# Kernel optimization log

Measured on AMD Instinct MI355X. Metric: run time of the kernel, lower is better.

Reference implementation:

```python
import jax, jax.numpy as jnp
import numpy as np

N, L, P = 8192, 20, 30          # obstacles, observation_len, pred_len
E, H, C = 64, 128, 2048         # embed_size, hidden_size, cnn_out_size (resnet50)


def setup_inputs() -> dict:
    key = jax.random.key(0)
    ks = jax.random.split(key, 10)
    rn = lambda k, s, sc=1.0: jax.random.normal(k, s, jnp.float32) * sc
    return {
        "img_embedding": rn(ks[0], (N, C)),
        "obs_pos": rn(ks[1], (N, L, 2)),
        "obs_pos_rel": rn(ks[2], (N, L, 2), 0.1),
        "obs_hist_size": jax.random.randint(ks[3], (N,), 0, L, jnp.int32),
        "h0": rn(ks[4], (H,), 0.1),
        "W_embed": rn(ks[5], (2, E), 0.5),
        "b_embed": jnp.zeros((E,), jnp.float32),
        "W_ih": rn(ks[6], (E, 4 * H), 1.0 / np.sqrt(E)),
        "W_hh": rn(ks[7], (H, 4 * H), 1.0 / np.sqrt(H)),
        "b_ih": jnp.zeros((4 * H,), jnp.float32),
        "b_hh": jnp.zeros((4 * H,), jnp.float32),
        "W_pred": rn(ks[8], (H + C, 2), 1.0 / np.sqrt(H + C)),
        "b_pred": jnp.zeros((2,), jnp.float32),
    }


def _forward(img_embedding, obs_pos, obs_pos_rel, obs_hist_size, h0,
             W_embed, b_embed, W_ih, W_hh, b_ih, b_hh, W_pred, b_pred):
    n, l, _ = obs_pos.shape
    hid = h0.shape[0]
    h = jnp.broadcast_to(h0, (n, hid))
    c = h  # original code initializes BOTH ht and ct from h0 (faithful to source)

    def lstm_cell(h, c, rel):
        # disp_embed (Linear(2,E)+ReLU) followed by a single LSTM step, PyTorch gate order i,f,g,o
        e = jax.nn.relu(rel @ W_embed + b_embed)            # [n, E]
        g = e @ W_ih + h @ W_hh + (b_ih + b_hh)             # [n, 4H]
        i, f, gg, o = jnp.split(g, 4, axis=-1)
        c_new = jax.nn.sigmoid(f) * c + jax.nn.sigmoid(i) * jnp.tanh(gg)
        h_new = jax.nn.sigmoid(o) * jnp.tanh(c_new)
        return h_new, c_new

    # ---- observation phase: t = 1 .. l-1, masked state update ----
    thresh = l - jnp.arange(1, l)                           # [l-1]
    masks = obs_hist_size[None, :] > thresh[:, None]        # [l-1, n] bool
    rels = jnp.swapaxes(obs_pos_rel[:, 1:, :], 0, 1)        # [l-1, n, 2]

    def obs_step(carry, x):
        h, c = carry
        rel, m = x
        h_new, c_new = lstm_cell(h, c, rel)
        m = m[:, None]
        return (jnp.where(m, h_new, h), jnp.where(m, c_new, c)), None

    (h, c), _ = jax.lax.scan(obs_step, (h, c), (rels, masks))

    # ---- prediction phase: pred_mask == all ones ----
    # pred_layer(cat(ht, img_emb)) == ht @ Wp_h + (img_emb @ Wp_img + b); the image
    # part is loop-invariant so hoist it (same math, far less memory traffic).
    img_proj = img_embedding @ W_pred[hid:] + b_pred        # [n, 2]
    Wp_h = W_pred[:hid]                                     # [H, 2]

    def pred_step(carry, _):
        h, c, pos = carry
        rel = h @ Wp_h + img_proj                           # pred_out[:, t-L]
        pos = pos + rel                                     # pred_traj[:, t-L]
        h_new, c_new = lstm_cell(h, c, rel)
        return (h_new, c_new, pos), pos

    _, traj = jax.lax.scan(pred_step, (h, c, obs_pos[:, -1, :]), None, length=P)
    return jnp.swapaxes(traj, 0, 1)                         # [n, P, 2]


def reference(img_embedding, obs_pos, obs_pos_rel, obs_hist_size, h0,
              W_embed, b_embed, W_ih, W_hh, b_ih, b_hh, W_pred, b_pred):
    return _forward(img_embedding, obs_pos, obs_pos_rel, obs_hist_size, h0,
                    W_embed, b_embed, W_ih, W_hh, b_ih, b_hh, W_pred, b_pred)
```

## Files before the change

kernel.cpp:

```cpp
#include <hip/hip_runtime.h>

typedef float f32x4 __attribute__((ext_vector_type(4)));
typedef float f32x2 __attribute__((ext_vector_type(2)));
typedef short bf16x8 __attribute__((ext_vector_type(8)));

#define N_TOT 8192
#define L_OBS 20
#define P_PRED 30
#define E_DIM 64
#define H_DIM 128
#define C_DIM 2048
#define G_DIM 512
#define M_ROWS 32
#define NTH 512
#define A_PAD 200

#define K1 1.442695041f
#define K2 2.885390082f

static __device__ __forceinline__ unsigned short f2bf(float f) {
  union { float f; unsigned int u; } v; v.f = f;
  unsigned int u = v.u;
  return (unsigned short)((u + 0x7FFFu + ((u >> 16) & 1u)) >> 16);
}
static __device__ __forceinline__ float bf2f(unsigned short b) {
  union { unsigned int u; float f; } v; v.u = ((unsigned int)b) << 16;
  return v.f;
}
static __device__ __forceinline__ float ex2(float x)  { float r; asm("v_exp_f32 %0, %1" : "=v"(r) : "v"(x)); return r; }
static __device__ __forceinline__ float rcpn(float x) { float r; asm("v_rcp_f32 %0, %1" : "=v"(r) : "v"(x)); return r; }
static __device__ __forceinline__ unsigned int cvtpk(float lo, float hi) {
  unsigned int r; asm("v_cvt_pk_bf16_f32 %0, %1, %2" : "=v"(r) : "v"(lo), "v"(hi)); return r;
}

__global__ __launch_bounds__(NTH, 2)
void lstm_traj(const float* __restrict__ img,
               const float* __restrict__ obs_pos,
               const float* __restrict__ obs_rel,
               const int*   __restrict__ hist,
               const float* __restrict__ h0,
               const float* __restrict__ W_embed,
               const float* __restrict__ b_embed,
               const float* __restrict__ W_ih,
               const float* __restrict__ W_hh,
               const float* __restrict__ b_ih,
               const float* __restrict__ b_hh,
               const float* __restrict__ W_pred,
               const float* __restrict__ b_pred,
               float* __restrict__ out)
{
  __shared__ unsigned short A_lds[2][M_ROWS][A_PAD];
  __shared__ float We_lds[2][E_DIM];
  __shared__ float be_lds[E_DIM];
  __shared__ float Wp_lds[H_DIM][2];

  const int t    = threadIdx.x;
  const int w    = t >> 6;
  const int l    = t & 63;
  const int u15  = l & 15;
  const int rq   = l >> 4;
  const int u    = w * 16 + u15;
  const int wg0  = blockIdx.x * M_ROWS;
  const int grow = t >> 4;
  const int gj   = t & 15;

  const float* relrow = obs_rel + (wg0 + grow) * (L_OBS * 2);

  if (t < 128) We_lds[t >> 6][t & 63] = W_embed[t];
  if (t < 64)  be_lds[t] = b_embed[t];
  if (t >= 128 && t < 384) ((float*)Wp_lds)[t - 128] = W_pred[t - 128];
  __syncthreads();

  bf16x8 B[4][6];
#pragma unroll
  for (int ks = 0; ks < 6; ++ks)
#pragma unroll
    for (int i = 0; i < 8; ++i) {
      const int k = ks * 32 + rq * 8 + i;
      const float* Wrow = (k < E_DIM) ? (W_ih + k * G_DIM) : (W_hh + (k - E_DIM) * G_DIM);
#pragma unroll
      for (int gt = 0; gt < 4; ++gt)
        B[gt][ks][i] = (short)f2bf(Wrow[gt * 128 + u]);
    }

  const float nbi = -K1 * (b_ih[u]       + b_hh[u]);
  const float nbf = -K1 * (b_ih[128 + u] + b_hh[128 + u]);
  const float nbg = -K2 * (b_ih[256 + u] + b_hh[256 + u]);
  const float nbo = -K1 * (b_ih[384 + u] + b_hh[384 + u]);

  const float h0u = h0[u];
  const unsigned short h0b = f2bf(h0u);
  float hf[2][4];
  float cs[2][4];
  int sact[2];
#pragma unroll
  for (int rt = 0; rt < 2; ++rt) {
    sact[rt] = 0;
#pragma unroll
    for (int q = 0; q < 4; ++q) {
      const int row = rt * 16 + rq * 4 + q;
      hf[rt][q] = h0u; cs[rt][q] = h0u;
      sact[rt] |= ((20 - hist[wg0 + row]) & 255) << (8 * q);
      A_lds[0][row][64 + u] = h0b;
    }
  }

  {
    const f32x2 rr = *(const f32x2*)(relrow + 2 * 2);
    const int j = gj * 4;
    const float e0 = fmaxf(fmaf(rr.x, We_lds[0][j],     fmaf(rr.y, We_lds[1][j],     be_lds[j])),     0.f);
    const float e1 = fmaxf(fmaf(rr.x, We_lds[0][j + 1], fmaf(rr.y, We_lds[1][j + 1], be_lds[j + 1])), 0.f);
    const float e2 = fmaxf(fmaf(rr.x, We_lds[0][j + 2], fmaf(rr.y, We_lds[1][j + 2], be_lds[j + 2])), 0.f);
    const float e3 = fmaxf(fmaf(rr.x, We_lds[0][j + 3], fmaf(rr.y, We_lds[1][j + 3], be_lds[j + 3])), 0.f);
    uint2 pk; pk.x = cvtpk(e0, e1); pk.y = cvtpk(e2, e3);
    *(uint2*)&A_lds[0][grow][j] = pk;
  }

  float pos0 = obs_pos[(wg0 + grow) * (L_OBS * 2) + (L_OBS - 1) * 2];
  float pos1 = obs_pos[(wg0 + grow) * (L_OBS * 2) + (L_OBS - 1) * 2 + 1];
  float ip0 = 0.f, ip1 = 0.f;
  {
    const float* irow = img + (long)(wg0 + grow) * C_DIM;
#pragma unroll 4
    for (int i = 0; i < 32; ++i) {
      const int k0 = i * 64 + gj * 4;
      const f32x4 v  = *(const f32x4*)(irow + k0);
      const f32x4 wa = *(const f32x4*)(W_pred + (H_DIM + k0) * 2);
      const f32x4 wb = *(const f32x4*)(W_pred + (H_DIM + k0) * 2 + 4);
      ip0 = fmaf(v.x, wa.x, fmaf(v.y, wa.z, fmaf(v.z, wb.x, fmaf(v.w, wb.z, ip0))));
      ip1 = fmaf(v.x, wa.y, fmaf(v.y, wa.w, fmaf(v.z, wb.y, fmaf(v.w, wb.w, ip1))));
    }
#pragma unroll
    for (int m = 8; m >= 1; m >>= 1) { ip0 += __shfl_xor(ip0, m); ip1 += __shfl_xor(ip1, m); }
    ip0 += b_pred[0]; ip1 += b_pred[1];
  }
  __syncthreads();

  int cur = 0;

  auto gates_and_h = [&](f32x4 (&acc)[2][4], int nxt_, int s_, bool domask) {
#pragma unroll
    for (int rt = 0; rt < 2; ++rt) {
#pragma unroll
      for (int q = 0; q < 4; ++q) {
        const float A_ = ex2(fmaf(acc[rt][0][q], -K1, nbi));
        const float F_ = ex2(fmaf(acc[rt][1][q], -K1, nbf));
        const float B_ = ex2(fmaf(acc[rt][2][q], -K2, nbg));
        const float C_ = ex2(fmaf(acc[rt][3][q], -K1, nbo));
        const float P2 = 1.f + B_;
        const float PB = (1.f + A_) * P2;
        const float Q  = 1.f + F_;
        const float cn = fmaf(cs[rt][q], PB, (2.f - P2) * Q) * rcpn(PB * Q);
        const float D_ = ex2(-K2 * cn);
        const float tc = fmaf(2.f, rcpn(1.f + D_), -1.f);
        const float hn = tc * rcpn(1.f + C_);
        bool act = true;
        if (domask) act = s_ >= ((sact[rt] >> (8 * q)) & 255);
        if (act) { cs[rt][q] = cn; hf[rt][q] = hn; }
      }
      const unsigned int p01 = cvtpk(hf[rt][0], hf[rt][1]);
      const unsigned int p23 = cvtpk(hf[rt][2], hf[rt][3]);
      const int rowb = rt * 16 + rq * 4;
      A_lds[nxt_][rowb + 0][64 + u] = (unsigned short)p01;
      A_lds[nxt_][rowb + 1][64 + u] = (unsigned short)(p01 >> 16);
      A_lds[nxt_][rowb + 2][64 + u] = (unsigned short)p23;
      A_lds[nxt_][rowb + 3][64 + u] = (unsigned short)(p23 >> 16);
    }
  };

#pragma unroll 1
  for (int s = 1; s < L_OBS - 1; ++s) {
    const int nxt = cur ^ 1;
    const int sN = (s + 2 <= L_OBS - 1) ? (s + 2) : (L_OBS - 1);
    const f32x2 rrN = *(const f32x2*)(relrow + sN * 2);

    f32x4 acc[2][4];
#pragma unroll
    for (int rt = 0; rt < 2; ++rt)
#pragma unroll
      for (int gt = 0; gt < 4; ++gt) { acc[rt][gt].x = 0.f; acc[rt][gt].y = 0.f; acc[rt][gt].z = 0.f; acc[rt][gt].w = 0.f; }
#pragma unroll
    for (int ks = 0; ks < 6; ++ks)
#pragma unroll
      for (int rt = 0; rt < 2; ++rt) {
        const bf16x8 a = *(const bf16x8*)&A_lds[cur][rt * 16 + u15][ks * 32 + rq * 8];
#pragma unroll
        for (int gt = 0; gt < 4; ++gt)
          acc[rt][gt] = __builtin_amdgcn_mfma_f32_16x16x32_bf16(a, B[gt][ks], acc[rt][gt], 0, 0, 0);
      }

    {
      const int j = gj * 4;
      const float e0 = fmaxf(fmaf(rrN.x, We_lds[0][j],     fmaf(rrN.y, We_lds[1][j],     be_lds[j])),     0.f);
      const float e1 = fmaxf(fmaf(rrN.x, We_lds[0][j + 1], fmaf(rrN.y, We_lds[1][j + 1], be_lds[j + 1])), 0.f);
      const float e2 = fmaxf(fmaf(rrN.x, We_lds[0][j + 2], fmaf(rrN.y, We_lds[1][j + 2], be_lds[j + 2])), 0.f);
      const float e3 = fmaxf(fmaf(rrN.x, We_lds[0][j + 3], fmaf(rrN.y, We_lds[1][j + 3], be_lds[j + 3])), 0.f);
      uint2 pk; pk.x = cvtpk(e0, e1); pk.y = cvtpk(e2, e3);
      *(uint2*)&A_lds[nxt][grow][j] = pk;
    }

    gates_and_h(acc, nxt, s, true);
    cur = nxt;
    __syncthreads();
  }

#pragma unroll 1
  for (int p = 0; p < P_PRED; ++p) {
    f32x4 acc[2][4];
    const bool last = (p == P_PRED - 1);
    if (!last) {
#pragma unroll
      for (int rt = 0; rt < 2; ++rt)
#pragma unroll
        for (int gt = 0; gt < 4; ++gt) { acc[rt][gt].x = 0.f; acc[rt][gt].y = 0.f; acc[rt][gt].z = 0.f; acc[rt][gt].w = 0.f; }
#pragma unroll
      for (int ks = 2; ks < 6; ++ks)
#pragma unroll
        for (int rt = 0; rt < 2; ++rt) {
          const bf16x8 a = *(const bf16x8*)&A_lds[cur][rt * 16 + u15][ks * 32 + rq * 8];
#pragma unroll
          for (int gt = 0; gt < 4; ++gt)
            acc[rt][gt] = __builtin_amdgcn_mfma_f32_16x16x32_bf16(a, B[gt][ks], acc[rt][gt], 0, 0, 0);
        }
    }

    const bf16x8 hv = *(const bf16x8*)&A_lds[cur][grow][64 + gj * 8];
    float s0 = 0.f, s1 = 0.f;
#pragma unroll
    for (int i = 0; i < 8; ++i) {
      const float hfv = bf2f((unsigned short)hv[i]);
      s0 = fmaf(hfv, Wp_lds[gj * 8 + i][0], s0);
      s1 = fmaf(hfv, Wp_lds[gj * 8 + i][1], s1);
    }
#pragma unroll
    for (int m = 8; m >= 1; m >>= 1) { s0 += __shfl_xor(s0, m); s1 += __shfl_xor(s1, m); }
    const float rel0 = s0 + ip0, rel1 = s1 + ip1;
    pos0 += rel0; pos1 += rel1;
    if (gj == 0) {
      float2 o; o.x = pos0; o.y = pos1;
      *(float2*)&out[((long)(wg0 + grow) * P_PRED + p) * 2] = o;
    }
    if (last) break;

    {
      const int j = gj * 4;
      const float e0 = fmaxf(fmaf(rel0, We_lds[0][j],     fmaf(rel1, We_lds[1][j],     be_lds[j])),     0.f);
      const float e1 = fmaxf(fmaf(rel0, We_lds[0][j + 1], fmaf(rel1, We_lds[1][j + 1], be_lds[j + 1])), 0.f);
      const float e2 = fmaxf(fmaf(rel0, We_lds[0][j + 2], fmaf(rel1, We_lds[1][j + 2], be_lds[j + 2])), 0.f);
      const float e3 = fmaxf(fmaf(rel0, We_lds[0][j + 3], fmaf(rel1, We_lds[1][j + 3], be_lds[j + 3])), 0.f);
      uint2 pk; pk.x = cvtpk(e0, e1); pk.y = cvtpk(e2, e3);
      *(uint2*)&A_lds[cur][grow][j] = pk;
    }
    __syncthreads();

#pragma unroll
    for (int ks = 0; ks < 2; ++ks)
#pragma unroll
      for (int rt = 0; rt < 2; ++rt) {
        const bf16x8 a = *(const bf16x8*)&A_lds[cur][rt * 16 + u15][ks * 32 + rq * 8];
#pragma unroll
        for (int gt = 0; gt < 4; ++gt)
          acc[rt][gt] = __builtin_amdgcn_mfma_f32_16x16x32_bf16(a, B[gt][ks], acc[rt][gt], 0, 0, 0);
      }

    const int nxt = cur ^ 1;
    gates_and_h(acc, nxt, 0, false);
    cur = nxt;
    __syncthreads();
  }
}

extern "C" void kernel_launch(void* const* d_in, const int* in_sizes, int n_in,
                              void* d_out, int out_size, void* d_ws, size_t ws_size,
                              hipStream_t stream) {
  (void)in_sizes; (void)n_in; (void)out_size; (void)d_ws; (void)ws_size;
  lstm_traj<<<dim3(N_TOT / M_ROWS), dim3(NTH), 0, stream>>>(
      (const float*)d_in[0],
      (const float*)d_in[1],
      (const float*)d_in[2],
      (const int*)  d_in[3],
      (const float*)d_in[4],
      (const float*)d_in[5],
      (const float*)d_in[6],
      (const float*)d_in[7],
      (const float*)d_in[8],
      (const float*)d_in[9],
      (const float*)d_in[10],
      (const float*)d_in[11],
      (const float*)d_in[12],
      (float*)d_out);
}
```

Baseline: 125.0 us.

## Compute prediction projection via MFMA in registers, drop mid-step barrier

The prediction-phase output projection h@Wp_h now runs as small MFMAs against a register-resident bf16 copy of W_pred, with results broadcast by ds_bpermute, instead of an LDS scalar dot plus shuffle reduction. Each wave then computes its own embedding fragments for the input part in registers. This removes the LDS write and the __syncthreads between embedding and the input-side MFMAs in every prediction step. In exchange it adds redundant per-wave embedding compute and more register pressure (wpf, ah, ef) under a 2-blocks-per-CU launch bound.

```diff
diff --git a/kernel.cpp b/kernel.cpp
--- a/kernel.cpp
+++ b/kernel.cpp
@@ -23,14 +23,13 @@
   unsigned int u = v.u;
   return (unsigned short)((u + 0x7FFFu + ((u >> 16) & 1u)) >> 16);
 }
-static __device__ __forceinline__ float bf2f(unsigned short b) {
-  union { unsigned int u; float f; } v; v.u = ((unsigned int)b) << 16;
-  return v.f;
-}
 static __device__ __forceinline__ float ex2(float x)  { float r; asm("v_exp_f32 %0, %1" : "=v"(r) : "v"(x)); return r; }
 static __device__ __forceinline__ float rcpn(float x) { float r; asm("v_rcp_f32 %0, %1" : "=v"(r) : "v"(x)); return r; }
 static __device__ __forceinline__ unsigned int cvtpk(float lo, float hi) {
   unsigned int r; asm("v_cvt_pk_bf16_f32 %0, %1, %2" : "=v"(r) : "v"(lo), "v"(hi)); return r;
+}
+static __device__ __forceinline__ float bperm16(int u15, float v) {
+  return __int_as_float(__builtin_amdgcn_ds_bpermute(u15 << 2, __float_as_int(v)));
 }
 
 __global__ __launch_bounds__(NTH, 2)
@@ -52,7 +51,7 @@
   __shared__ unsigned short A_lds[2][M_ROWS][A_PAD];
   __shared__ float We_lds[2][E_DIM];
   __shared__ float be_lds[E_DIM];
-  __shared__ float Wp_lds[H_DIM][2];
+  __shared__ float ip_lds[M_ROWS][2];
 
   const int t    = threadIdx.x;
   const int w    = t >> 6;
@@ -68,7 +67,6 @@
 
   if (t < 128) We_lds[t >> 6][t & 63] = W_embed[t];
   if (t < 64)  be_lds[t] = b_embed[t];
-  if (t >= 128 && t < 384) ((float*)Wp_lds)[t - 128] = W_pred[t - 128];
   __syncthreads();
 
   bf16x8 B[4][6];
@@ -81,6 +79,15 @@
 #pragma unroll
       for (int gt = 0; gt < 4; ++gt)
         B[gt][ks][i] = (short)f2bf(Wrow[gt * 128 + u]);
+    }
+
+  bf16x8 wpf[4];
+#pragma unroll
+  for (int ks4 = 0; ks4 < 4; ++ks4)
+#pragma unroll
+    for (int i = 0; i < 8; ++i) {
+      const int k = ks4 * 32 + rq * 8 + i;
+      wpf[ks4][i] = (u15 < 2) ? (short)f2bf(W_pred[k * 2 + u15]) : (short)0;
     }
 
   const float nbi = -K1 * (b_ih[u]       + b_hh[u]);
@@ -116,10 +123,8 @@
     *(uint2*)&A_lds[0][grow][j] = pk;
   }
 
-  float pos0 = obs_pos[(wg0 + grow) * (L_OBS * 2) + (L_OBS - 1) * 2];
-  float pos1 = obs_pos[(wg0 + grow) * (L_OBS * 2) + (L_OBS - 1) * 2 + 1];
-  float ip0 = 0.f, ip1 = 0.f;
   {
+    float ig0 = 0.f, ig1 = 0.f;
     const float* irow = img + (long)(wg0 + grow) * C_DIM;
 #pragma unroll 4
     for (int i = 0; i < 32; ++i) {
@@ -127,14 +132,21 @@
       const f32x4 v  = *(const f32x4*)(irow + k0);
       const f32x4 wa = *(const f32x4*)(W_pred + (H_DIM + k0) * 2);
       const f32x4 wb = *(const f32x4*)(W_pred + (H_DIM + k0) * 2 + 4);
-      ip0 = fmaf(v.x, wa.x, fmaf(v.y, wa.z, fmaf(v.z, wb.x, fmaf(v.w, wb.z, ip0))));
-      ip1 = fmaf(v.x, wa.y, fmaf(v.y, wa.w, fmaf(v.z, wb.y, fmaf(v.w, wb.w, ip1))));
-    }
-#pragma unroll
-    for (int m = 8; m >= 1; m >>= 1) { ip0 += __shfl_xor(ip0, m); ip1 += __shfl_xor(ip1, m); }
-    ip0 += b_pred[0]; ip1 += b_pred[1];
+      ig0 = fmaf(v.x, wa.x, fmaf(v.y, wa.z, fmaf(v.z, wb.x, fmaf(v.w, wb.z, ig0))));
+      ig1 = fmaf(v.x, wa.y, fmaf(v.y, wa.w, fmaf(v.z, wb.y, fmaf(v.w, wb.w, ig1))));
+    }
+#pragma unroll
+    for (int m = 8; m >= 1; m >>= 1) { ig0 += __shfl_xor(ig0, m); ig1 += __shfl_xor(ig1, m); }
+    if (gj == 0) { ip_lds[grow][0] = ig0 + b_pred[0]; ip_lds[grow][1] = ig1 + b_pred[1]; }
   }
   __syncthreads();
+
+  const float ipA0 = ip_lds[u15][0],      ipA1 = ip_lds[u15][1];
+  const float ipB0 = ip_lds[16 + u15][0], ipB1 = ip_lds[16 + u15][1];
+  float posA0 = obs_pos[(wg0 + u15) * (L_OBS * 2) + (L_OBS - 1) * 2];
+  float posA1 = obs_pos[(wg0 + u15) * (L_OBS * 2) + (L_OBS - 1) * 2 + 1];
+  float posB0 = obs_pos[(wg0 + 16 + u15) * (L_OBS * 2) + (L_OBS - 1) * 2];
+  float posB1 = obs_pos[(wg0 + 16 + u15) * (L_OBS * 2) + (L_OBS - 1) * 2 + 1];
 
   int cur = 0;
 
@@ -206,62 +218,79 @@
 
 #pragma unroll 1
   for (int p = 0; p < P_PRED; ++p) {
+    const bool last = (p == P_PRED - 1);
+
+    bf16x8 ah[2][4];
+#pragma unroll
+    for (int rt = 0; rt < 2; ++rt)
+#pragma unroll
+      for (int ks4 = 0; ks4 < 4; ++ks4)
+        ah[rt][ks4] = *(const bf16x8*)&A_lds[cur][rt * 16 + u15][64 + ks4 * 32 + rq * 8];
+
+    f32x4 racc[2];
+#pragma unroll
+    for (int rt = 0; rt < 2; ++rt) {
+      racc[rt].x = 0.f; racc[rt].y = 0.f; racc[rt].z = 0.f; racc[rt].w = 0.f;
+#pragma unroll
+      for (int ks4 = 0; ks4 < 4; ++ks4)
+        racc[rt] = __builtin_amdgcn_mfma_f32_16x16x32_bf16(wpf[ks4], ah[rt][ks4], racc[rt], 0, 0, 0);
+    }
+
     f32x4 acc[2][4];
-    const bool last = (p == P_PRED - 1);
     if (!last) {
 #pragma unroll
       for (int rt = 0; rt < 2; ++rt)
 #pragma unroll
         for (int gt = 0; gt < 4; ++gt) { acc[rt][gt].x = 0.f; acc[rt][gt].y = 0.f; acc[rt][gt].z = 0.f; acc[rt][gt].w = 0.f; }
 #pragma unroll
-      for (int ks = 2; ks < 6; ++ks)
-#pragma unroll
-        for (int rt = 0; rt < 2; ++rt) {
-          const bf16x8 a = *(const bf16x8*)&A_lds[cur][rt * 16 + u15][ks * 32 + rq * 8];
+      for (int ks4 = 0; ks4 < 4; ++ks4)
+#pragma unroll
+        for (int rt = 0; rt < 2; ++rt)
 #pragma unroll
           for (int gt = 0; gt < 4; ++gt)
-            acc[rt][gt] = __builtin_amdgcn_mfma_f32_16x16x32_bf16(a, B[gt][ks], acc[rt][gt], 0, 0, 0);
+            acc[rt][gt] = __builtin_amdgcn_mfma_f32_16x16x32_bf16(ah[rt][ks4], B[gt][ks4 + 2], acc[rt][gt], 0, 0, 0);
+    }
+
+    const float relA0 = bperm16(u15, racc[0].x) + ipA0;
+    const float relA1 = bperm16(u15, racc[0].y) + ipA1;
+    const float relB0 = bperm16(u15, racc[1].x) + ipB0;
+    const float relB1 = bperm16(u15, racc[1].y) + ipB1;
+    posA0 += relA0; posA1 += relA1;
+    posB0 += relB0; posB1 += relB1;
+    if (rq == 0) {
+      float2 oA; oA.x = posA0; oA.y = posA1;
+      float2 oB; oB.x = posB0; oB.y = posB1;
+      *(float2*)&out[((long)(wg0 + u15) * P_PRED + p) * 2]      = oA;
+      *(float2*)&out[((long)(wg0 + 16 + u15) * P_PRED + p) * 2] = oB;
+    }
+    if (last) break;
+
+    bf16x8 ef[2][2];
+#pragma unroll
+    for (int rt = 0; rt < 2; ++rt) {
+      const float r0 = rt ? relB0 : relA0;
+      const float r1 = rt ? relB1 : relA1;
+#pragma unroll
+      for (int kb = 0; kb < 2; ++kb) {
+        union { unsigned int uu[4]; bf16x8 v; } pk;
+#pragma unroll
+        for (int ii = 0; ii < 4; ++ii) {
+          const int k0 = kb * 32 + rq * 8 + 2 * ii;
+          const float ea = fmaxf(fmaf(r0, We_lds[0][k0],     fmaf(r1, We_lds[1][k0],     be_lds[k0])),     0.f);
+          const float eb = fmaxf(fmaf(r0, We_lds[0][k0 + 1], fmaf(r1, We_lds[1][k0 + 1], be_lds[k0 + 1])), 0.f);
+          pk.uu[ii] = cvtpk(ea, eb);
         }
-    }
-
-    const bf16x8 hv = *(const bf16x8*)&A_lds[cur][grow][64 + gj * 8];
-    float s0 = 0.f, s1 = 0.f;
-#pragma unroll
-    for (int i = 0; i < 8; ++i) {
-      const float hfv = bf2f((unsigned short)hv[i]);
-      s0 = fmaf(hfv, Wp_lds[gj * 8 + i][0], s0);
-      s1 = fmaf(hfv, Wp_lds[gj * 8 + i][1], s1);
-    }
-#pragma unroll
-    for (int m = 8; m >= 1; m >>= 1) { s0 += __shfl_xor(s0, m); s1 += __shfl_xor(s1, m); }
-    const float rel0 = s0 + ip0, rel1 = s1 + ip1;
-    pos0 += rel0; pos1 += rel1;
-    if (gj == 0) {
-      float2 o; o.x = pos0; o.y = pos1;
-      *(float2*)&out[((long)(wg0 + grow) * P_PRED + p) * 2] = o;
-    }
-    if (last) break;
-
-    {
-      const int j = gj * 4;
-      const float e0 = fmaxf(fmaf(rel0, We_lds[0][j],     fmaf(rel1, We_lds[1][j],     be_lds[j])),     0.f);
-      const float e1 = fmaxf(fmaf(rel0, We_lds[0][j + 1], fmaf(rel1, We_lds[1][j + 1], be_lds[j + 1])), 0.f);
-      const float e2 = fmaxf(fmaf(rel0, We_lds[0][j + 2], fmaf(rel1, We_lds[1][j + 2], be_lds[j + 2])), 0.f);
-      const float e3 = fmaxf(fmaf(rel0, We_lds[0][j + 3], fmaf(rel1, We_lds[1][j + 3], be_lds[j + 3])), 0.f);
-      uint2 pk; pk.x = cvtpk(e0, e1); pk.y = cvtpk(e2, e3);
-      *(uint2*)&A_lds[cur][grow][j] = pk;
-    }
-    __syncthreads();
-
-#pragma unroll
-    for (int ks = 0; ks < 2; ++ks)
-#pragma unroll
-      for (int rt = 0; rt < 2; ++rt) {
-        const bf16x8 a = *(const bf16x8*)&A_lds[cur][rt * 16 + u15][ks * 32 + rq * 8];
+        ef[rt][kb] = pk.v;
+      }
+    }
+
+#pragma unroll
+    for (int kb = 0; kb < 2; ++kb)
+#pragma unroll
+      for (int rt = 0; rt < 2; ++rt)
 #pragma unroll
         for (int gt = 0; gt < 4; ++gt)
-          acc[rt][gt] = __builtin_amdgcn_mfma_f32_16x16x32_bf16(a, B[gt][ks], acc[rt][gt], 0, 0, 0);
-      }
+          acc[rt][gt] = __builtin_amdgcn_mfma_f32_16x16x32_bf16(ef[rt][kb], B[gt][kb], acc[rt][gt], 0, 0, 0);
 
     const int nxt = cur ^ 1;
     gates_and_h(acc, nxt, 0, false);
```

Result: slower. 138.1 us (+10.5%).
